# Kernel optimization log

Hardware: AMD Instinct MI355X
Metric: run time of the kernel (lower is better)

Reference implementation:

```python
import jax, jax.numpy as jnp
import numpy as np

N_BLOCKS = 16
N_HEADS = 2
HEAD_DIM = 32
SCALE = HEAD_DIM ** (-0.5)


def setup_inputs() -> dict:
    key = jax.random.key(0)
    ks = jax.random.split(key, 5)
    b, s, d = 16, 4096, 1024
    nb, bd = N_BLOCKS, 1024 // N_BLOCKS  # block_dim = 64; emb per-block dim = 64
    w_std = 1.0 / np.sqrt(bd)
    inp = {
        'x': jax.random.normal(ks[0], (b, s, d), dtype=jnp.float32),
        'wq': jax.random.normal(ks[1], (nb, bd, bd), dtype=jnp.float32) * w_std,
        'bq': jnp.zeros((nb, bd), dtype=jnp.float32),
        'wk': jax.random.normal(ks[2], (nb, bd, bd), dtype=jnp.float32) * w_std,
        'bk': jnp.zeros((nb, bd), dtype=jnp.float32),
        'wv': jax.random.normal(ks[3], (nb, bd, bd), dtype=jnp.float32) * w_std,
        'bv': jnp.zeros((nb, bd), dtype=jnp.float32),
        'wf': jax.random.normal(ks[4], (nb, bd, bd), dtype=jnp.float32) * w_std,
        'bf': jnp.zeros((nb, bd), dtype=jnp.float32),
    }
    return inp


def _group_linear(x, w, b):
    # x: [B, S, G*I] -> per-block linear -> [B, S, G*O]
    B, S, _ = x.shape
    G, I, O = w.shape
    xg = x.reshape(B, S, G, I)
    y = jnp.einsum('bsgi,gio->bsgo', xg, w) + b
    return y.reshape(B, S, G * O)


def reference(x, wq, bq, wk, bk, wv, bv, wf, bf):
    B, S, D = x.shape
    nb, nh, hd = N_BLOCKS, N_HEADS, HEAD_DIM
    # grouped QKV projections -> [B, S, nb, nh, hd] -> heads before blocks
    q = _group_linear(x, wq, bq).reshape(B, S, nb, nh, hd).transpose(0, 1, 3, 2, 4) * SCALE
    k = _group_linear(x, wk, bk).reshape(B, S, nb, nh, hd).transpose(0, 1, 3, 2, 4)
    v = _group_linear(x, wv, bv).reshape(B, S, nb, nh, hd).transpose(0, 1, 3, 2, 4)
    # attention across blocks: score [B, S, nh, nb, nb]
    score = jnp.einsum('bshgd,bshfd->bshgf', q, k)
    score = jax.nn.softmax(score, axis=-1)
    out = jnp.einsum('bshgf,bshfd->bshgd', score, v)
    # back to [B, S, nb, nh, hd] then flatten
    out = out.transpose(0, 1, 3, 2, 4).reshape(B, S, nb * nh * hd)
    out = _group_linear(out, wf, bf)
    return out.reshape(B, S, D)
```

## Files before the change

kernel.cpp:

```cpp
#include <hip/hip_runtime.h>
#include <hip/hip_bf16.h>
#include <stdint.h>


typedef __attribute__((ext_vector_type(8))) short bf16x8;
typedef __attribute__((ext_vector_type(4))) float f32x4;

#define NTOK   65536
#define DM     1024
#define TT     32
#define QSCALE 0.17677669529663687f
#define LOG2E  1.4426950408889634f

static __device__ __forceinline__ unsigned short f2bf(float f) {
  union { __hip_bfloat16 h; unsigned short s; } cv;
  cv.h = __float2bfloat16(f);
  return cv.s;
}

static __device__ __forceinline__ unsigned int pk2(float a, float b) {
  return (unsigned int)f2bf(a) | ((unsigned int)f2bf(b) << 16);
}

static __device__ __forceinline__ bf16x8 pack8(float4 a, float4 b) {
  bf16x8 r;
  r[0] = (short)f2bf(a.x); r[1] = (short)f2bf(a.y);
  r[2] = (short)f2bf(a.z); r[3] = (short)f2bf(a.w);
  r[4] = (short)f2bf(b.x); r[5] = (short)f2bf(b.y);
  r[6] = (short)f2bf(b.z); r[7] = (short)f2bf(b.w);
  return r;
}

union FragCast { uint4 u4; bf16x8 v; uint2 u2[2]; unsigned int u[4]; };

__global__ void build_wfrag(const float* __restrict__ wq, const float* __restrict__ wk,
                            const float* __restrict__ wv, const float* __restrict__ wf,
                            uint4* __restrict__ wfrag) {
  int tid = blockIdx.x * 256 + threadIdx.x;
  if (tid >= 4 * 16 * 2 * 4 * 64) return;
  int lane =  tid        & 63;
  int nf   = (tid >> 6)  & 3;
  int kk   = (tid >> 8)  & 1;
  int g    = (tid >> 9)  & 15;
  int mat  =  tid >> 13;
  const float* w = (mat == 0) ? wq : (mat == 1) ? wk : (mat == 2) ? wv : wf;
  float sc = (mat == 0) ? QSCALE : 1.0f;
  int o  = nf * 16 + (lane & 15);
  int kb = kk * 32 + 8 * (lane >> 4);
  unsigned int packed[4];
#pragma unroll
  for (int jj = 0; jj < 4; ++jj) {
    unsigned short lo = f2bf(w[(g * 64 + kb + 2 * jj    ) * 64 + o] * sc);
    unsigned short hi = f2bf(w[(g * 64 + kb + 2 * jj + 1) * 64 + o] * sc);
    packed[jj] = (unsigned int)lo | ((unsigned int)hi << 16);
  }
  uint4 u; u.x = packed[0]; u.y = packed[1]; u.z = packed[2]; u.w = packed[3];
  wfrag[tid] = u;
}


#define QK_STORE(fA_, fB_, nf2_, h_, bp_, bsc_, dst_) do {                    \
  const int nf = 2 * (h_) + (nf2_);                                           \
  float4 b4 = *(const float4*)&(bp_)[g * 64 + nf * 16 + 4 * lq];              \
  _Pragma("unroll")                                                           \
  for (int m = 0; m < 2; ++m) {                                               \
    f32x4 a1 = {b4.x * (bsc_), b4.y * (bsc_), b4.z * (bsc_), b4.w * (bsc_)};  \
    a1 = __builtin_amdgcn_mfma_f32_16x16x32_bf16((fA_).v, afr[m][0], a1, 0, 0, 0); \
    a1 = __builtin_amdgcn_mfma_f32_16x16x32_bf16((fB_).v, afr[m][1], a1, 0, 0, 0); \
    uint2 w2; w2.x = pk2(a1[0], a1[1]); w2.y = pk2(a1[2], a1[3]);             \
    const int blk = (16 * (2 * (nf2_) + (lq >> 1)) + g) ^ (lr & 7);           \
    *(uint2*)&(dst_)[(16 * m + lr) * 512 + blk * 8 + 4 * (lq & 1)] = w2;      \
  }                                                                           \
} while (0)

#define V_STORE(fA_, fB_, nf2_, h_) do {                                      \
  const int nf = 2 * (h_) + (nf2_);                                           \
  const float bias = bv[g * 64 + nf * 16 + lr];                               \
  const int L = 16 * (g >> 2) + lr;                                           \
  const int jj = g & 3;                                                       \
  _Pragma("unroll")                                                           \
  for (int m = 0; m < 2; ++m) {                                               \
    f32x4 a1 = {bias, bias, bias, bias};                                      \
    a1 = __builtin_amdgcn_mfma_f32_16x16x32_bf16(afr[m][0], (fA_).v, a1, 0, 0, 0); \
    a1 = __builtin_amdgcn_mfma_f32_16x16x32_bf16(afr[m][1], (fB_).v, a1, 0, 0, 0); \
    _Pragma("unroll")                                                         \
    for (int r = 0; r < 4; ++r)                                               \
      s_v[((16 * m + 4 * lq + r) * 2 + (nf2_)) * 256 + L * 4 + jj] = f2bf(a1[r]); \
  }                                                                           \
} while (0)

#define PH1(h_) do {                                                          \
  FragCast q0a, q0b, q1a, q1b, k0a, k0b, k1a, k1b, v0a, v0b, v1a, v1b;        \
  q0a.u4 = wfrag[(((0 * 16 + g) * 2 + 0) * 4 + 2 * (h_)    ) * 64 + lane];    \
  q0b.u4 = wfrag[(((0 * 16 + g) * 2 + 1) * 4 + 2 * (h_)    ) * 64 + lane];    \
  q1a.u4 = wfrag[(((0 * 16 + g) * 2 + 0) * 4 + 2 * (h_) + 1) * 64 + lane];    \
  q1b.u4 = wfrag[(((0 * 16 + g) * 2 + 1) * 4 + 2 * (h_) + 1) * 64 + lane];    \
  k0a.u4 = wfrag[(((1 * 16 + g) * 2 + 0) * 4 + 2 * (h_)    ) * 64 + lane];    \
  k0b.u4 = wfrag[(((1 * 16 + g) * 2 + 1) * 4 + 2 * (h_)    ) * 64 + lane];    \
  k1a.u4 = wfrag[(((1 * 16 + g) * 2 + 0) * 4 + 2 * (h_) + 1) * 64 + lane];    \
  k1b.u4 = wfrag[(((1 * 16 + g) * 2 + 1) * 4 + 2 * (h_) + 1) * 64 + lane];    \
  v0a.u4 = wfrag[(((2 * 16 + g) * 2 + 0) * 4 + 2 * (h_)    ) * 64 + lane];    \
  v0b.u4 = wfrag[(((2 * 16 + g) * 2 + 1) * 4 + 2 * (h_)    ) * 64 + lane];    \
  v1a.u4 = wfrag[(((2 * 16 + g) * 2 + 0) * 4 + 2 * (h_) + 1) * 64 + lane];    \
  v1b.u4 = wfrag[(((2 * 16 + g) * 2 + 1) * 4 + 2 * (h_) + 1) * 64 + lane];    \
  QK_STORE(q0a, q0b, 0, h_, bq, QSCALE, s_q);                                 \
  QK_STORE(q1a, q1b, 1, h_, bq, QSCALE, s_q);                                 \
  QK_STORE(k0a, k0b, 0, h_, bk, 1.0f,   s_k);                                 \
  QK_STORE(k1a, k1b, 1, h_, bk, 1.0f,   s_k);                                 \
  V_STORE(v0a, v0b, 0, h_);                                                   \
  V_STORE(v1a, v1b, 1, h_);                                                   \
} while (0)

#define PH2(ATT_) do {                                                        \
  _Pragma("unroll")                                                           \
  for (int tt = 0; tt < 2; ++tt) {                                            \
    const int t = g + 16 * tt;                                                \
    f32x4 zero = {0.f, 0.f, 0.f, 0.f};                                        \
    FragCast qa, ka;                                                          \
    const int blk = lane ^ (t & 7);                                           \
    qa.u4 = *(const uint4*)&s_q[t * 512 + blk * 8];                           \
    ka.u4 = *(const uint4*)&s_k[t * 512 + blk * 8];                           \
                  \
    f32x4 sc4 = __builtin_amdgcn_mfma_f32_16x16x32_bf16(ka.v, qa.v, zero, 0, 0, 0); \
    float m = fmaxf(fmaxf(sc4[0], sc4[1]), fmaxf(sc4[2], sc4[3]));            \
    m = fmaxf(m, __shfl_xor(m, 16));                                          \
    m = fmaxf(m, __shfl_xor(m, 32));                                          \
    float p0 = exp2f((sc4[0] - m) * LOG2E);                                   \
    float p1 = exp2f((sc4[1] - m) * LOG2E);                                   \
    float p2 = exp2f((sc4[2] - m) * LOG2E);                                   \
    float p3 = exp2f((sc4[3] - m) * LOG2E);                                   \
    float s = p0 + p1 + p2 + p3;                                              \
    s += __shfl_xor(s, 16);                                                   \
    s += __shfl_xor(s, 32);                                                   \
    const float inv = __fdividef(1.0f, s);                                    \
    FragCast pa;                      \
    pa.u[0] = pk2(p0 * inv, p1 * inv);                                        \
    pa.u[1] = pk2(p2 * inv, p3 * inv);                                        \
    pa.u[2] = 0; pa.u[3] = 0;                                                 \
    FragCast va0, va1;          \
    va0.u2[0] = *(const uint2*)&s_v[(t * 2 + 0) * 256 + lane * 4];            \
    va0.u[2] = 0; va0.u[3] = 0;                                               \
    va1.u2[0] = *(const uint2*)&s_v[(t * 2 + 1) * 256 + lane * 4];            \
    va1.u[2] = 0; va1.u[3] = 0;                                               \
                                   \
    f32x4 oo0 = __builtin_amdgcn_mfma_f32_16x16x32_bf16(va0.v, pa.v, zero, 0, 0, 0); \
    f32x4 oo1 = __builtin_amdgcn_mfma_f32_16x16x32_bf16(va1.v, pa.v, zero, 0, 0, 0); \
    uint2 w20; w20.x = pk2(oo0[0], oo0[1]); w20.y = pk2(oo0[2], oo0[3]);      \
    const int ab0 = (16 * (0 + (lq >> 1)) + lr) ^ (t & 7);                    \
    *(uint2*)&(ATT_)[t * 512 + ab0 * 8 + 4 * (lq & 1)] = w20;                 \
    uint2 w21; w21.x = pk2(oo1[0], oo1[1]); w21.y = pk2(oo1[2], oo1[3]);      \
    const int ab1 = (16 * (2 + (lq >> 1)) + lr) ^ (t & 7);                    \
    *(uint2*)&(ATT_)[t * 512 + ab1 * 8 + 4 * (lq & 1)] = w21;                 \
  }                                                                           \
} while (0)

#define LOADF() do {                                                          \
  f0n0.u4 = wfrag[(((3 * 16 + g) * 2 + 0) * 4 + 0) * 64 + lane];              \
  f0n1.u4 = wfrag[(((3 * 16 + g) * 2 + 0) * 4 + 1) * 64 + lane];              \
  f0n2.u4 = wfrag[(((3 * 16 + g) * 2 + 0) * 4 + 2) * 64 + lane];              \
  f0n3.u4 = wfrag[(((3 * 16 + g) * 2 + 0) * 4 + 3) * 64 + lane];              \
  f1n0.u4 = wfrag[(((3 * 16 + g) * 2 + 1) * 4 + 0) * 64 + lane];              \
  f1n1.u4 = wfrag[(((3 * 16 + g) * 2 + 1) * 4 + 1) * 64 + lane];              \
  f1n2.u4 = wfrag[(((3 * 16 + g) * 2 + 1) * 4 + 2) * 64 + lane];              \
  f1n3.u4 = wfrag[(((3 * 16 + g) * 2 + 1) * 4 + 3) * 64 + lane];              \
} while (0)

#define PH3_NF(f0_, f1_, nf_, m_, aa0_, aa1_) do {                            \
  float4 b4 = *(const float4*)&bfb[g * 64 + (nf_) * 16 + 4 * lq];             \
  f32x4 a1 = {b4.x, b4.y, b4.z, b4.w};                                        \
  a1 = __builtin_amdgcn_mfma_f32_16x16x32_bf16((f0_).v, (aa0_).v, a1, 0, 0, 0); \
  a1 = __builtin_amdgcn_mfma_f32_16x16x32_bf16((f1_).v, (aa1_).v, a1, 0, 0, 0); \
  float4 o4; o4.x = a1[0]; o4.y = a1[1]; o4.z = a1[2]; o4.w = a1[3];          \
  *(float4*)&out[(tok0 + 16 * (m_) + lr) * DM + g * 64 + (nf_) * 16 + 4 * lq] = o4; \
} while (0)

#define PH3() do {                                                            \
  const int blk3 = (16 * lq + g) ^ (lr & 7);                                  \
  _Pragma("unroll")                                                           \
  for (int m = 0; m < 2; ++m) {                                               \
    FragCast aa0, aa1;             \
    aa0.u4 = *(const uint4*)&s_a0[(16 * m + lr) * 512 + blk3 * 8];            \
    aa1.u4 = *(const uint4*)&s_a1[(16 * m + lr) * 512 + blk3 * 8];            \
    PH3_NF(f0n0, f1n0, 0, m, aa0, aa1);                                       \
    PH3_NF(f0n1, f1n1, 1, m, aa0, aa1);                                       \
    PH3_NF(f0n2, f1n2, 2, m, aa0, aa1);                                       \
    PH3_NF(f0n3, f1n3, 3, m, aa0, aa1);                                       \
  }                                                                           \
} while (0)

__global__ __launch_bounds__(1024)
void fused_gc32(const float* __restrict__ x,
                const float* __restrict__ bq, const float* __restrict__ bk,
                const float* __restrict__ bv, const float* __restrict__ bfb,
                const uint4* __restrict__ wfrag,
                float* __restrict__ out) {
  extern __shared__ __align__(16) unsigned short sm[];
  unsigned short* const s_q  = sm;
  unsigned short* const s_k  = sm + 16384;
  unsigned short* const s_v  = sm + 32768;
  unsigned short* const s_a0 = sm + 49152;
  unsigned short* const s_a1 = sm + 65536;

  const int tid  = threadIdx.x;
  const int g    = tid >> 6;
  const int lane = tid & 63;
  const int lr   = lane & 15;
  const int lq   = lane >> 4;
  const long tok0 = (long)blockIdx.x * TT;

  bf16x8 afr[2][2];
#pragma unroll
  for (int m = 0; m < 2; ++m) {
    const float* xr = x + (tok0 + 16 * m + lr) * DM + g * 64;
#pragma unroll
    for (int kk = 0; kk < 2; ++kk) {
      const float* p = xr + kk * 32 + 8 * lq;
      afr[m][kk] = pack8(*(const float4*)p, *(const float4*)(p + 4));
    }
  }

  FragCast f0n0, f0n1, f0n2, f0n3, f1n0, f1n1, f1n2, f1n3;

  PH1(0);
  __syncthreads();
  PH2(s_a0);
  __syncthreads();
  PH1(1);
  __syncthreads();
  LOADF();
  PH2(s_a1);
  __syncthreads();
  PH3();
}

extern "C" void kernel_launch(void* const* d_in, const int* in_sizes, int n_in,
                              void* d_out, int out_size, void* d_ws, size_t ws_size,
                              hipStream_t stream) {
  const float* x   = (const float*)d_in[0];
  const float* wq  = (const float*)d_in[1];
  const float* bq_ = (const float*)d_in[2];
  const float* wk  = (const float*)d_in[3];
  const float* bk_ = (const float*)d_in[4];
  const float* wv  = (const float*)d_in[5];
  const float* bv_ = (const float*)d_in[6];
  const float* wf  = (const float*)d_in[7];
  const float* bf_ = (const float*)d_in[8];
  (void)in_sizes; (void)n_in; (void)out_size; (void)ws_size;

  uint4* wfrag = (uint4*)d_ws;

  static_assert(sizeof(unsigned short) == 2, "");
  const int lds_bytes = 5 * 32 * 1024;
  hipFuncSetAttribute(reinterpret_cast<const void*>(fused_gc32),
                      hipFuncAttributeMaxDynamicSharedMemorySize, lds_bytes);

  build_wfrag<<<128, 256, 0, stream>>>(wq, wk, wv, wf, wfrag);
  fused_gc32<<<NTOK / TT, 1024, lds_bytes, stream>>>(x, bq_, bk_, bv_, bf_,
                                                     wfrag, (float*)d_out);
}
```

Before: 193.0 us.

## Make fused kernel persistent over eight tiles with register prefetch of next x tile

Each block now loops over eight 32-token tiles instead of processing one, shrinking the grid to one block per CU. The next tile's x rows are loaded into registers in the middle of the current tile's work and packed to bf16 after the final phase. This is meant to hide global load latency for x and amortize block launch and prologue costs. It adds register pressure from the prefetch buffers and may leave CUs idle at the end if work is uneven.

```diff
diff --git a/kernel.cpp b/kernel.cpp
--- a/kernel.cpp
+++ b/kernel.cpp
@@ -8,7 +8,8 @@
 
 #define NTOK   65536
 #define DM     1024
-#define TT     32
+#define TILE   32
+#define NT     8
 #define QSCALE 0.17677669529663687f
 #define LOG2E  1.4426950408889634f
 
@@ -188,8 +189,28 @@
   }                                                                           \
 } while (0)
 
-__global__ __launch_bounds__(1024)
-void fused_gc32(const float* __restrict__ x,
+#define XLOAD(tokbase_) do {                                                  \
+  const float* xr0 = x + ((tokbase_) + lr) * DM + g * 64;                     \
+  xA0 = *(const float4*)(xr0 + 8 * lq);                                       \
+  xA1 = *(const float4*)(xr0 + 8 * lq + 4);                                   \
+  xA2 = *(const float4*)(xr0 + 32 + 8 * lq);                                  \
+  xA3 = *(const float4*)(xr0 + 32 + 8 * lq + 4);                              \
+  const float* xr1 = x + ((tokbase_) + 16 + lr) * DM + g * 64;                \
+  xB0 = *(const float4*)(xr1 + 8 * lq);                                       \
+  xB1 = *(const float4*)(xr1 + 8 * lq + 4);                                   \
+  xB2 = *(const float4*)(xr1 + 32 + 8 * lq);                                  \
+  xB3 = *(const float4*)(xr1 + 32 + 8 * lq + 4);                              \
+} while (0)
+
+#define XPACK() do {                                                          \
+  afr[0][0] = pack8(xA0, xA1);                                                \
+  afr[0][1] = pack8(xA2, xA3);                                                \
+  afr[1][0] = pack8(xB0, xB1);                                                \
+  afr[1][1] = pack8(xB2, xB3);                                                \
+} while (0)
+
+__global__ __launch_bounds__(1024, 4)
+void fused_pers(const float* __restrict__ x,
                 const float* __restrict__ bq, const float* __restrict__ bk,
                 const float* __restrict__ bv, const float* __restrict__ bfb,
                 const uint4* __restrict__ wfrag,
@@ -206,31 +227,33 @@
   const int lane = tid & 63;
   const int lr   = lane & 15;
   const int lq   = lane >> 4;
-  const long tok0 = (long)blockIdx.x * TT;
 
   bf16x8 afr[2][2];
-#pragma unroll
-  for (int m = 0; m < 2; ++m) {
-    const float* xr = x + (tok0 + 16 * m + lr) * DM + g * 64;
-#pragma unroll
-    for (int kk = 0; kk < 2; ++kk) {
-      const float* p = xr + kk * 32 + 8 * lq;
-      afr[m][kk] = pack8(*(const float4*)p, *(const float4*)(p + 4));
-    }
+  float4 xA0, xA1, xA2, xA3, xB0, xB1, xB2, xB3;
+  FragCast f0n0, f0n1, f0n2, f0n3, f1n0, f1n1, f1n2, f1n3;
+
+  const long base = (long)blockIdx.x * (NT * TILE);
+  XLOAD(base);
+  XPACK();
+
+  for (int it = 0; it < NT; ++it) {
+    const long tok0 = base + (long)it * TILE;
+
+    PH1(0);
+    __syncthreads();
+    PH2(s_a0);
+    __syncthreads();
+
+    if (it + 1 < NT) XLOAD(tok0 + TILE);
+
+    PH1(1);
+    __syncthreads();
+    LOADF();
+    PH2(s_a1);
+    __syncthreads();
+    PH3();
+    if (it + 1 < NT) XPACK();
   }
-
-  FragCast f0n0, f0n1, f0n2, f0n3, f1n0, f1n1, f1n2, f1n3;
-
-  PH1(0);
-  __syncthreads();
-  PH2(s_a0);
-  __syncthreads();
-  PH1(1);
-  __syncthreads();
-  LOADF();
-  PH2(s_a1);
-  __syncthreads();
-  PH3();
 }
 
 extern "C" void kernel_launch(void* const* d_in, const int* in_sizes, int n_in,
@@ -249,12 +272,11 @@
 
   uint4* wfrag = (uint4*)d_ws;
 
-  static_assert(sizeof(unsigned short) == 2, "");
   const int lds_bytes = 5 * 32 * 1024;
-  hipFuncSetAttribute(reinterpret_cast<const void*>(fused_gc32),
+  hipFuncSetAttribute(reinterpret_cast<const void*>(fused_pers),
                       hipFuncAttributeMaxDynamicSharedMemorySize, lds_bytes);
 
   build_wfrag<<<128, 256, 0, stream>>>(wq, wk, wv, wf, wfrag);
-  fused_gc32<<<NTOK / TT, 1024, lds_bytes, stream>>>(x, bq_, bk_, bv_, bf_,
-                                                     wfrag, (float*)d_out);
-}
+  fused_pers<<<NTOK / (NT * TILE), 1024, lds_bytes, stream>>>(
+      x, bq_, bk_, bv_, bf_, wfrag, (float*)d_out);
+}
```

Result: slower. 444.8 us (+130.5%).

## Make fused kernel loop over eight tiles and prefetch next tile's x

Applied to the files above, without the earlier changes.

Each block now handles eight consecutive 32-token tiles in a loop instead of one, which cuts the grid from 2048 to 256 blocks. While PH3 computes the current tile, the block loads the x rows for the next tile into registers and then packs them to bf16, overlapping global loads with compute. With 160KB of LDS per block there is one block per CU, so 256 blocks roughly match the CU count and launch overhead shrinks, but tail balance and register pressure from the prefetch buffers may get worse. PH3 still reads s_a1 while other waves may already be writing the next PH1, since the loop adds no barrier after PH3, which could be a race.

```diff
diff --git a/kernel.cpp b/kernel.cpp
--- a/kernel.cpp
+++ b/kernel.cpp
@@ -8,7 +8,8 @@
 
 #define NTOK   65536
 #define DM     1024
-#define TT     32
+#define TILE   32
+#define NT     8
 #define QSCALE 0.17677669529663687f
 #define LOG2E  1.4426950408889634f
 
@@ -188,12 +189,25 @@
   }                                                                           \
 } while (0)
 
+#define XLOAD_HALF(tokrow_) do {                                              \
+  const float* xr = x + (tokrow_) * DM + g * 64;                              \
+  y0 = *(const float4*)(xr + 8 * lq);                                         \
+  y1 = *(const float4*)(xr + 8 * lq + 4);                                     \
+  y2 = *(const float4*)(xr + 32 + 8 * lq);                                    \
+  y3 = *(const float4*)(xr + 32 + 8 * lq + 4);                                \
+} while (0)
+
+#define XPACK_HALF(m_) do {                                                   \
+  afr[m_][0] = pack8(y0, y1);                                                 \
+  afr[m_][1] = pack8(y2, y3);                                                 \
+} while (0)
+
 __global__ __launch_bounds__(1024)
-void fused_gc32(const float* __restrict__ x,
-                const float* __restrict__ bq, const float* __restrict__ bk,
-                const float* __restrict__ bv, const float* __restrict__ bfb,
-                const uint4* __restrict__ wfrag,
-                float* __restrict__ out) {
+void fused_pers32(const float* __restrict__ x,
+                  const float* __restrict__ bq, const float* __restrict__ bk,
+                  const float* __restrict__ bv, const float* __restrict__ bfb,
+                  const uint4* __restrict__ wfrag,
+                  float* __restrict__ out) {
   extern __shared__ __align__(16) unsigned short sm[];
   unsigned short* const s_q  = sm;
   unsigned short* const s_k  = sm + 16384;
@@ -206,31 +220,36 @@
   const int lane = tid & 63;
   const int lr   = lane & 15;
   const int lq   = lane >> 4;
-  const long tok0 = (long)blockIdx.x * TT;
+  const long base = (long)blockIdx.x * (NT * TILE);
 
   bf16x8 afr[2][2];
-#pragma unroll
-  for (int m = 0; m < 2; ++m) {
-    const float* xr = x + (tok0 + 16 * m + lr) * DM + g * 64;
-#pragma unroll
-    for (int kk = 0; kk < 2; ++kk) {
-      const float* p = xr + kk * 32 + 8 * lq;
-      afr[m][kk] = pack8(*(const float4*)p, *(const float4*)(p + 4));
+  float4 y0, y1, y2, y3;
+  FragCast f0n0, f0n1, f0n2, f0n3, f1n0, f1n1, f1n2, f1n3;
+
+  XLOAD_HALF(base + lr);       XPACK_HALF(0);
+  XLOAD_HALF(base + 16 + lr);  XPACK_HALF(1);
+
+  for (int it = 0; it < NT; ++it) {
+    const long tok0 = base + (long)it * TILE;
+
+    PH1(0);
+    __syncthreads();
+    PH2(s_a0);
+    __syncthreads();
+    PH1(1);
+    __syncthreads();
+    LOADF();
+    PH2(s_a1);
+    __syncthreads();
+
+    if (it + 1 < NT) XLOAD_HALF(tok0 + TILE + lr);
+    PH3();
+    if (it + 1 < NT) {
+      XPACK_HALF(0);
+      XLOAD_HALF(tok0 + TILE + 16 + lr);
+      XPACK_HALF(1);
     }
   }
-
-  FragCast f0n0, f0n1, f0n2, f0n3, f1n0, f1n1, f1n2, f1n3;
-
-  PH1(0);
-  __syncthreads();
-  PH2(s_a0);
-  __syncthreads();
-  PH1(1);
-  __syncthreads();
-  LOADF();
-  PH2(s_a1);
-  __syncthreads();
-  PH3();
 }
 
 extern "C" void kernel_launch(void* const* d_in, const int* in_sizes, int n_in,
@@ -249,12 +268,11 @@
 
   uint4* wfrag = (uint4*)d_ws;
 
-  static_assert(sizeof(unsigned short) == 2, "");
   const int lds_bytes = 5 * 32 * 1024;
-  hipFuncSetAttribute(reinterpret_cast<const void*>(fused_gc32),
+  hipFuncSetAttribute(reinterpret_cast<const void*>(fused_pers32),
                       hipFuncAttributeMaxDynamicSharedMemorySize, lds_bytes);
 
   build_wfrag<<<128, 256, 0, stream>>>(wq, wk, wv, wf, wfrag);
-  fused_gc32<<<NTOK / TT, 1024, lds_bytes, stream>>>(x, bq_, bk_, bv_, bf_,
-                                                     wfrag, (float*)d_out);
-}
+  fused_pers32<<<NTOK / (NT * TILE), 1024, lds_bytes, stream>>>(
+      x, bq_, bk_, bv_, bf_, wfrag, (float*)d_out);
+}
```

Measured after the change: 346.1 us. 1.79x slower.
